# Performance work log

Measured on AMD Instinct MI355X. Metric: run time of the kernel, lower is better.

The kernel has to match this reference:

```python
import jax, jax.numpy as jnp
import numpy as np

N_NODES = 20000
N_EDGES = 100000
WIDTH = 64
KER_IN = 6
KER_HID = WIDTH // 4  # 16
DEPTH = 6


def setup_inputs() -> dict:
    key = jax.random.key(0)
    ks = jax.random.split(key, 12)
    s = lambda fan_in: 1.0 / np.sqrt(fan_in)
    return {
        "x": jax.random.normal(ks[0], (N_NODES, 1), dtype=jnp.float32),
        "edge_index": jax.random.randint(ks[1], (2, N_EDGES), 0, N_NODES, dtype=jnp.int32),
        "edge_attr": jax.random.uniform(ks[2], (N_EDGES, KER_IN), dtype=jnp.float32),
        "fc1_w": jax.random.normal(ks[3], (1, WIDTH), dtype=jnp.float32) * s(1),
        "fc1_b": jnp.zeros((WIDTH,), dtype=jnp.float32),
        "k1_w": jax.random.normal(ks[4], (KER_IN, KER_HID), dtype=jnp.float32) * s(KER_IN),
        "k1_b": jnp.zeros((KER_HID,), dtype=jnp.float32),
        "k2_w": jax.random.normal(ks[5], (KER_HID, WIDTH * WIDTH), dtype=jnp.float32) * s(KER_HID),
        "k2_b": jnp.zeros((WIDTH * WIDTH,), dtype=jnp.float32),
        "root_w": jax.random.normal(ks[6], (WIDTH, WIDTH), dtype=jnp.float32) * s(WIDTH),
        "conv_b": jnp.zeros((WIDTH,), dtype=jnp.float32),
        "fc2_w": jax.random.normal(ks[7], (WIDTH, 1), dtype=jnp.float32) * s(WIDTH),
        "fc2_b": jnp.zeros((1,), dtype=jnp.float32),
    }


def reference(x, edge_index, edge_attr, fc1_w, fc1_b, k1_w, k1_b, k2_w, k2_b,
              root_w, conv_b, fc2_w, fc2_b):
    src = edge_index[0]  # source nodes j
    dst = edge_index[1]  # target nodes i

    # fc1: lift node features [N,1] -> [N,W]
    h = x @ fc1_w + fc1_b

    # Edge-conditioned weight matrices via kernel MLP (edge_attr is layer-invariant,
    # so compute once and reuse for all DEPTH layers — identical math).
    ek = jax.nn.relu(edge_attr @ k1_w + k1_b)           # [E, W/4]
    W = (ek @ k2_w + k2_b).reshape(N_EDGES, WIDTH, WIDTH)  # [E, W, W]

    # mean aggregation denominator (in-degree, clamped to avoid div-by-zero)
    deg = jax.ops.segment_sum(jnp.ones((N_EDGES,), dtype=h.dtype), dst,
                              num_segments=N_NODES)
    denom = jnp.maximum(deg, 1.0)[:, None]               # [N,1]

    for _ in range(DEPTH):
        # per-edge matmul: msg_e = x_src[e] @ W_e
        msg = jnp.einsum('ei,eio->eo', h[src], W)        # [E, W]
        agg = jax.ops.segment_sum(msg, dst, num_segments=N_NODES) / denom
        h = jax.nn.relu(agg + h @ root_w + conv_b)       # NNConv root weight + bias, then outer ReLU

    return h @ fc2_w + fc2_b                              # [N, 1]
```

## Files before the change

kernel.cpp:

```cpp
#include <hip/hip_runtime.h>
#include <hip/hip_bf16.h>


#define NN 20000
#define NE 100000
#define WD 64
#define DEPTH 6
#define TM 15
#define LSTR 1092

typedef __attribute__((ext_vector_type(8))) short bf16x8;
typedef __attribute__((ext_vector_type(4))) float f32x4;

__device__ __forceinline__ unsigned short f2bf(float v) {
    union { float f; unsigned u; } x; x.f = v;
    unsigned r = x.u + 0x7fffu + ((x.u >> 16) & 1u);
    return (unsigned short)(r >> 16);
}
__device__ __forceinline__ float bf2f(unsigned short b) {
    union { unsigned u; float f; } x; x.u = ((unsigned)b) << 16;
    return x.f;
}

__global__ __launch_bounds__(256) void count_kernel(const int* __restrict__ ei,
                                                    int* __restrict__ outc,
                                                    int* __restrict__ inc)
{
    int e = blockIdx.x * 256 + threadIdx.x;
    if (e >= NE) return;
    atomicAdd(&outc[ei[e]], 1);
    atomicAdd(&inc[ei[NE + e]], 1);
}

__global__ __launch_bounds__(256) void scanA_kernel(const int* __restrict__ cnt,
                                                    int* __restrict__ partials)
{
    int b = blockIdx.x, t = threadIdx.x, lane = t & 63, w = t >> 6;
    int base = b * 1024 + t * 4;
    int s = 0;
#pragma unroll
    for (int i = 0; i < 4; ++i) {
        int idx = base + i;
        if (idx < 2 * NN) s += cnt[idx];
    }
#pragma unroll
    for (int off = 32; off > 0; off >>= 1) s += __shfl_down(s, off, 64);
    __shared__ int wsum[4];
    if (lane == 0) wsum[w] = s;
    __syncthreads();
    if (t == 0) partials[b] = wsum[0] + wsum[1] + wsum[2] + wsum[3];
}

__global__ __launch_bounds__(64) void scanB_kernel(const int* __restrict__ partials,
                                                   int* __restrict__ bases)
{
    int l = threadIdx.x;
    int p = (l < 40) ? partials[l] : 0;
    int v = p;
#pragma unroll
    for (int off = 1; off < 64; off <<= 1) {
        int u = __shfl_up(v, off, 64);
        if (l >= off) v += u;
    }
    if (l < 40) bases[l] = v - p;
}

__global__ __launch_bounds__(256) void scanC_kernel(const int* __restrict__ cnt,
                                                    const int* __restrict__ bases,
                                                    int* __restrict__ rps,
                                                    int* __restrict__ rpd,
                                                    float* __restrict__ invd)
{
    int b = blockIdx.x, t = threadIdx.x, lane = t & 63, w = t >> 6;
    int base = b * 1024 + t * 4;
    int v[4], s = 0;
#pragma unroll
    for (int i = 0; i < 4; ++i) {
        int idx = base + i;
        v[i] = (idx < 2 * NN) ? cnt[idx] : 0;
        s += v[i];
    }
    int tsum = s, sc = s;
#pragma unroll
    for (int off = 1; off < 64; off <<= 1) {
        int u = __shfl_up(sc, off, 64);
        if (lane >= off) sc += u;
    }
    __shared__ int wtot[4];
    if (lane == 63) wtot[w] = sc;
    __syncthreads();
    int wbase = 0;
    for (int j = 0; j < w; ++j) wbase += wtot[j];
    int run = bases[b] + wbase + sc - tsum;
#pragma unroll
    for (int i = 0; i < 4; ++i) {
        int idx = base + i;
        int e = run; run += v[i];
        if (idx < NN) {
            rps[idx] = e;
        } else if (idx < 2 * NN) {
            rpd[idx - NN] = e - NE;
            invd[idx - NN] = 1.0f / fmaxf((float)v[i], 1.0f);
        }
    }
    if (b == 0 && t == 0) { rps[NN] = NE; rpd[NN] = NE; }
}

__global__ __launch_bounds__(256) void ekfill_kernel(
    const int* __restrict__ ei, const float* __restrict__ ea,
    const float* __restrict__ k1w, const float* __restrict__ k1b,
    const int* __restrict__ rps, const int* __restrict__ rpd,
    int* __restrict__ fs, int* __restrict__ fd,
    float* __restrict__ eks, int* __restrict__ ss2sd)
{
    int e = blockIdx.x * 256 + threadIdx.x;
    if (e >= NE) return;
    int s = ei[e], d = ei[NE + e];
    float a[6];
#pragma unroll
    for (int i = 0; i < 6; ++i) a[i] = ea[e * 6 + i];
    int slot_s = rps[s] + atomicAdd(&fs[s], 1);
    int slot_d = rpd[d] + atomicAdd(&fd[d], 1);
    ss2sd[slot_s] = slot_d;
#pragma unroll
    for (int j = 0; j < 16; ++j) {
        float v = k1b[j];
#pragma unroll
        for (int i = 0; i < 6; ++i) v = fmaf(a[i], k1w[i * 16 + j], v);
        eks[(size_t)slot_s * 16 + j] = fmaxf(v, 0.f);
    }
}

__global__ __launch_bounds__(256) void gwt_kernel(
    const float* __restrict__ k2w, const float* __restrict__ k2b,
    const float* __restrict__ rootw,
    unsigned short* __restrict__ Gh, unsigned short* __restrict__ Gl)
{
    int idx = blockIdx.x * 256 + threadIdx.x;
    if (idx >= 1152 * 64) return;
    int n = idx >> 6, k = idx & 63;
    int b = n >> 6, o = n & 63;
    float g;
    if (b < 16)       g = k2w[b * 4096 + k * 64 + o];
    else if (b == 16) g = k2b[k * 64 + o];
    else              g = rootw[k * 64 + o];
    unsigned short hi = f2bf(g);
    Gh[idx] = hi;
    Gl[idx] = f2bf(g - bf2f(hi));
}

__global__ __launch_bounds__(256) void h0_kernel(
    const float* __restrict__ x, const float* __restrict__ w,
    const float* __restrict__ b,
    unsigned short* __restrict__ hhi, unsigned short* __restrict__ hlo)
{
    int idx = blockIdx.x * 256 + threadIdx.x;
    if (idx >= NN * WD) return;
    int n = idx >> 6, o = idx & 63;
    float v = fmaf(x[n], w[o], b[o]);
    unsigned short hi = f2bf(v);
    hhi[idx] = hi;
    hlo[idx] = f2bf(v - bf2f(hi));
}

__global__ __launch_bounds__(512) void fused_kernel(
    const unsigned short* __restrict__ hhi, const unsigned short* __restrict__ hlo,
    const unsigned short* __restrict__ Gh, const unsigned short* __restrict__ Gl,
    const float* __restrict__ eks, const int* __restrict__ ss2sd,
    const int* __restrict__ rps, float* __restrict__ Proot,
    float* __restrict__ msg)
{
    __shared__ __align__(16) float Pt[TM * LSTR];
    __shared__ int rb[TM + 1];
    int n0 = blockIdx.x * TM;
    int w = threadIdx.x >> 6, l = threadIdx.x & 63;
    int quad = l >> 4, lr = l & 15;
    if (threadIdx.x < TM + 1) {
        int gi = n0 + threadIdx.x;
        rb[threadIdx.x] = rps[gi > NN ? NN : gi];
    }
    int arow = n0 + lr;
    if (arow > NN - 1) arow = NN - 1;
    const bf16x8* pah = (const bf16x8*)(hhi + (size_t)arow * 64 + quad * 8);
    const bf16x8* pal = (const bf16x8*)(hlo + (size_t)arow * 64 + quad * 8);
    bf16x8 ah0 = pah[0], ah1 = pah[4];
    bf16x8 al0 = pal[0], al1 = pal[4];

    for (int st = w; st < 18; st += 8) {
        f32x4 acc[4];
#pragma unroll
        for (int t = 0; t < 4; ++t) acc[t] = (f32x4){0.f, 0.f, 0.f, 0.f};
#pragma unroll
        for (int t = 0; t < 4; ++t) {
            int brow = st * 64 + t * 16 + lr;
            const bf16x8* pbh = (const bf16x8*)(Gh + (size_t)brow * 64 + quad * 8);
            const bf16x8* pbl = (const bf16x8*)(Gl + (size_t)brow * 64 + quad * 8);
            bf16x8 bh0 = pbh[0], bh1 = pbh[4];
            bf16x8 bl0 = pbl[0], bl1 = pbl[4];
            f32x4 a = acc[t];
            a = __builtin_amdgcn_mfma_f32_16x16x32_bf16(ah0, bh0, a, 0, 0, 0);
            a = __builtin_amdgcn_mfma_f32_16x16x32_bf16(ah0, bl0, a, 0, 0, 0);
            a = __builtin_amdgcn_mfma_f32_16x16x32_bf16(al0, bh0, a, 0, 0, 0);
            a = __builtin_amdgcn_mfma_f32_16x16x32_bf16(ah1, bh1, a, 0, 0, 0);
            a = __builtin_amdgcn_mfma_f32_16x16x32_bf16(ah1, bl1, a, 0, 0, 0);
            a = __builtin_amdgcn_mfma_f32_16x16x32_bf16(al1, bh1, a, 0, 0, 0);
            acc[t] = a;
        }
        if (st < 17) {
#pragma unroll
            for (int t = 0; t < 4; ++t)
#pragma unroll
                for (int r = 0; r < 4; ++r) {
                    int row = quad * 4 + r;
                    if (row < TM)
                        Pt[row * LSTR + st * 64 + t * 16 + lr] = acc[t][r];
                }
        } else {
#pragma unroll
            for (int t = 0; t < 4; ++t)
#pragma unroll
                for (int r = 0; r < 4; ++r) {
                    int row = quad * 4 + r;
                    int gn = n0 + row;
                    if (row < TM && gn < NN)
                        Proot[(size_t)gn * 64 + t * 16 + lr] = acc[t][r];
                }
        }
    }
    __syncthreads();

    int nend = n0 + TM; if (nend > NN) nend = NN;
    int r0 = rb[0], r1 = rb[nend - n0];
    int total = r1 - r0;
    if (total <= 0) return;
    int per = (total + 7) >> 3;
    int s0 = r0 + w * per;
    int s1 = s0 + per; if (s1 > r1) s1 = r1;
    int ln = 0;
    float p[17];
    bool need = true;
    for (int s = s0; s < s1; ++s) {
        while (s >= rb[ln + 1]) { ++ln; need = true; }
        if (need) {
            const float* Pr = &Pt[ln * LSTR];
#pragma unroll
            for (int k = 0; k < 17; ++k) p[k] = Pr[k * 64 + l];
            need = false;
        }
        int su = __builtin_amdgcn_readfirstlane(s);
        const float* er = eks + (size_t)su * 16;
        f32x4 e0 = *(const f32x4*)(er);
        f32x4 e1 = *(const f32x4*)(er + 4);
        f32x4 e2 = *(const f32x4*)(er + 8);
        f32x4 e3 = *(const f32x4*)(er + 12);
        int ds = ss2sd[su];
        float ma = p[16], mb = 0.f;
        ma = fmaf(e0[0], p[0], ma);  mb = fmaf(e0[1], p[1], mb);
        ma = fmaf(e0[2], p[2], ma);  mb = fmaf(e0[3], p[3], mb);
        ma = fmaf(e1[0], p[4], ma);  mb = fmaf(e1[1], p[5], mb);
        ma = fmaf(e1[2], p[6], ma);  mb = fmaf(e1[3], p[7], mb);
        ma = fmaf(e2[0], p[8], ma);  mb = fmaf(e2[1], p[9], mb);
        ma = fmaf(e2[2], p[10], ma); mb = fmaf(e2[3], p[11], mb);
        ma = fmaf(e3[0], p[12], ma); mb = fmaf(e3[1], p[13], mb);
        ma = fmaf(e3[2], p[14], ma); mb = fmaf(e3[3], p[15], mb);
        msg[(size_t)ds * 64 + l] = ma + mb;
    }
}

__global__ __launch_bounds__(256) void agg_kernel(
    const float* __restrict__ msg, const int* __restrict__ rpd,
    const float* __restrict__ invd, const float* __restrict__ Proot,
    const float* __restrict__ convb, float* __restrict__ h,
    unsigned short* __restrict__ hhi, unsigned short* __restrict__ hlo)
{
    int i = blockIdx.x * 4 + (threadIdx.x >> 6);
    if (i >= NN) return;
    int l = threadIdx.x & 63;
    int r0 = rpd[i], r1 = rpd[i + 1];
    float a0 = 0.f, a1 = 0.f, a2 = 0.f, a3 = 0.f;
    int s = r0;
    for (; s + 3 < r1; s += 4) {
        a0 += msg[(size_t)s * 64 + l];
        a1 += msg[(size_t)(s + 1) * 64 + l];
        a2 += msg[(size_t)(s + 2) * 64 + l];
        a3 += msg[(size_t)(s + 3) * 64 + l];
    }
    for (; s < r1; ++s) a0 += msg[(size_t)s * 64 + l];
    float acc = (a0 + a1) + (a2 + a3);
    float v = fmaf(acc, invd[i], Proot[(size_t)i * 64 + l] + convb[l]);
    v = fmaxf(v, 0.f);
    int idx = i * 64 + l;
    h[idx] = v;
    unsigned short hi = f2bf(v);
    hhi[idx] = hi;
    hlo[idx] = f2bf(v - bf2f(hi));
}

__global__ __launch_bounds__(256) void out_kernel(
    const float* __restrict__ h, const float* __restrict__ fc2_w,
    const float* __restrict__ fc2_b, float* __restrict__ out)
{
    int wave = blockIdx.x * 4 + (threadIdx.x >> 6);
    int lane = threadIdx.x & 63;
    float v = h[(size_t)wave * 64 + lane] * fc2_w[lane];
#pragma unroll
    for (int off = 32; off > 0; off >>= 1) v += __shfl_down(v, off);
    if (lane == 0) out[wave] = v + fc2_b[0];
}

extern "C" void kernel_launch(void* const* d_in, const int* in_sizes, int n_in,
                              void* d_out, int out_size, void* d_ws, size_t ws_size,
                              hipStream_t stream)
{
    const float* x         = (const float*)d_in[0];
    const int*   ei        = (const int*)  d_in[1];
    const float* edge_attr = (const float*)d_in[2];
    const float* fc1_w     = (const float*)d_in[3];
    const float* fc1_b     = (const float*)d_in[4];
    const float* k1_w      = (const float*)d_in[5];
    const float* k1_b      = (const float*)d_in[6];
    const float* k2_w      = (const float*)d_in[7];
    const float* k2_b      = (const float*)d_in[8];
    const float* root_w    = (const float*)d_in[9];
    const float* conv_b    = (const float*)d_in[10];
    const float* fc2_w     = (const float*)d_in[11];
    const float* fc2_b     = (const float*)d_in[12];
    float* out = (float*)d_out;

    float* ws = (float*)d_ws;
    size_t off = 0;
    int* cnt   = (int*)(ws + off); off += 4 * NN;
    int* outc  = cnt;
    int* inc   = cnt + NN;
    int* fs    = cnt + 2 * NN;
    int* fd    = cnt + 3 * NN;
    int* rps   = (int*)(ws + off); off += 20004;
    int* rpd   = (int*)(ws + off); off += 20004;
    int* partials = (int*)(ws + off); off += 64;
    int* bases    = (int*)(ws + off); off += 64;
    int* ss2sd    = (int*)(ws + off); off += NE;
    float* invd  = ws + off; off += NN;
    float* eks   = ws + off; off += (size_t)NE * 16;
    unsigned short* Gh  = (unsigned short*)(ws + off); off += 36864;
    unsigned short* Gl  = (unsigned short*)(ws + off); off += 36864;
    unsigned short* hhi = (unsigned short*)(ws + off); off += (size_t)NN * 32;
    unsigned short* hlo = (unsigned short*)(ws + off); off += (size_t)NN * 32;
    float* h     = ws + off; off += (size_t)NN * WD;
    float* msg   = ws + off; off += (size_t)NE * WD;
    float* Proot = ws + off; off += (size_t)NN * WD;

    hipMemsetAsync(cnt, 0, 4 * NN * sizeof(int), stream);
    count_kernel<<<(NE + 255) / 256, 256, 0, stream>>>(ei, outc, inc);
    scanA_kernel<<<40, 256, 0, stream>>>(cnt, partials);
    scanB_kernel<<<1, 64, 0, stream>>>(partials, bases);
    scanC_kernel<<<40, 256, 0, stream>>>(cnt, bases, rps, rpd, invd);
    ekfill_kernel<<<(NE + 255) / 256, 256, 0, stream>>>(ei, edge_attr, k1_w, k1_b,
                                                        rps, rpd, fs, fd, eks, ss2sd);
    gwt_kernel<<<(1152 * 64 + 255) / 256, 256, 0, stream>>>(k2_w, k2_b, root_w, Gh, Gl);
    h0_kernel<<<(NN * WD + 255) / 256, 256, 0, stream>>>(x, fc1_w, fc1_b, hhi, hlo);

    int ntiles = (NN + TM - 1) / TM;
    for (int layer = 0; layer < DEPTH; ++layer) {
        fused_kernel<<<ntiles, 512, 0, stream>>>(hhi, hlo, Gh, Gl, eks, ss2sd,
                                                 rps, Proot, msg);
        agg_kernel<<<(NN + 3) / 4, 256, 0, stream>>>(msg, rpd, invd, Proot,
                                                     conv_b, h, hhi, hlo);
    }

    out_kernel<<<NN / 4, 256, 0, stream>>>(h, fc2_w, fc2_b, out);
}
```

Before: 561.8 us.

## Replace CSR gather aggregation with atomic scatter and fuse node update into conv kernel

Drops the per-edge message buffer and the separate destination-sorted aggregation kernel. Messages are now atomically added straight into a per-layer agg buffer, and the next layer's fused kernel computes the ReLU node update and bf16 hi/lo split on the fly. The h0 kernel is folded into the first layer and the final update into out_kernel. This saves the msg write/read traffic and a launch per layer, at the cost of float atomics (nondeterministic summation order), an extra memset per layer, and ping-pong buffers.

```diff
diff --git a/kernel.cpp b/kernel.cpp
--- a/kernel.cpp
+++ b/kernel.cpp
@@ -68,7 +68,6 @@
 __global__ __launch_bounds__(256) void scanC_kernel(const int* __restrict__ cnt,
                                                     const int* __restrict__ bases,
                                                     int* __restrict__ rps,
-                                                    int* __restrict__ rpd,
                                                     float* __restrict__ invd)
 {
     int b = blockIdx.x, t = threadIdx.x, lane = t & 63, w = t >> 6;
@@ -99,19 +98,17 @@
         if (idx < NN) {
             rps[idx] = e;
         } else if (idx < 2 * NN) {
-            rpd[idx - NN] = e - NE;
             invd[idx - NN] = 1.0f / fmaxf((float)v[i], 1.0f);
         }
     }
-    if (b == 0 && t == 0) { rps[NN] = NE; rpd[NN] = NE; }
+    if (b == 0 && t == 0) rps[NN] = NE;
 }
 
 __global__ __launch_bounds__(256) void ekfill_kernel(
     const int* __restrict__ ei, const float* __restrict__ ea,
     const float* __restrict__ k1w, const float* __restrict__ k1b,
-    const int* __restrict__ rps, const int* __restrict__ rpd,
-    int* __restrict__ fs, int* __restrict__ fd,
-    float* __restrict__ eks, int* __restrict__ ss2sd)
+    const int* __restrict__ rps, int* __restrict__ fs,
+    float* __restrict__ eks, int* __restrict__ dsts)
 {
     int e = blockIdx.x * 256 + threadIdx.x;
     if (e >= NE) return;
@@ -120,8 +117,7 @@
 #pragma unroll
     for (int i = 0; i < 6; ++i) a[i] = ea[e * 6 + i];
     int slot_s = rps[s] + atomicAdd(&fs[s], 1);
-    int slot_d = rpd[d] + atomicAdd(&fd[d], 1);
-    ss2sd[slot_s] = slot_d;
+    dsts[slot_s] = d;
 #pragma unroll
     for (int j = 0; j < 16; ++j) {
         float v = k1b[j];
@@ -149,26 +145,15 @@
     Gl[idx] = f2bf(g - bf2f(hi));
 }
 
-__global__ __launch_bounds__(256) void h0_kernel(
-    const float* __restrict__ x, const float* __restrict__ w,
-    const float* __restrict__ b,
-    unsigned short* __restrict__ hhi, unsigned short* __restrict__ hlo)
-{
-    int idx = blockIdx.x * 256 + threadIdx.x;
-    if (idx >= NN * WD) return;
-    int n = idx >> 6, o = idx & 63;
-    float v = fmaf(x[n], w[o], b[o]);
-    unsigned short hi = f2bf(v);
-    hhi[idx] = hi;
-    hlo[idx] = f2bf(v - bf2f(hi));
-}
-
-__global__ __launch_bounds__(512) void fused_kernel(
-    const unsigned short* __restrict__ hhi, const unsigned short* __restrict__ hlo,
+__global__ __launch_bounds__(512, 4) void fused_kernel(
+    const float* __restrict__ x, const float* __restrict__ fc1w,
+    const float* __restrict__ fc1b,
+    const float* __restrict__ aggIn, const float* __restrict__ ProotIn,
+    const float* __restrict__ invd, const float* __restrict__ convb,
     const unsigned short* __restrict__ Gh, const unsigned short* __restrict__ Gl,
-    const float* __restrict__ eks, const int* __restrict__ ss2sd,
-    const int* __restrict__ rps, float* __restrict__ Proot,
-    float* __restrict__ msg)
+    const float* __restrict__ eks, const int* __restrict__ dsts,
+    const int* __restrict__ rps,
+    float* __restrict__ ProotOut, float* __restrict__ aggOut, int first)
 {
     __shared__ __align__(16) float Pt[TM * LSTR];
     __shared__ int rb[TM + 1];
@@ -181,10 +166,58 @@
     }
     int arow = n0 + lr;
     if (arow > NN - 1) arow = NN - 1;
-    const bf16x8* pah = (const bf16x8*)(hhi + (size_t)arow * 64 + quad * 8);
-    const bf16x8* pal = (const bf16x8*)(hlo + (size_t)arow * 64 + quad * 8);
-    bf16x8 ah0 = pah[0], ah1 = pah[4];
-    bf16x8 al0 = pal[0], al1 = pal[4];
+
+    bf16x8 ah0, al0, ah1, al1;
+    if (first) {
+        float xv = x[arow];
+#pragma unroll
+        for (int half = 0; half < 2; ++half) {
+            int kb = half * 32 + quad * 8;
+            f32x4 w0 = *(const f32x4*)(fc1w + kb);
+            f32x4 w1 = *(const f32x4*)(fc1w + kb + 4);
+            f32x4 b0 = *(const f32x4*)(fc1b + kb);
+            f32x4 b1 = *(const f32x4*)(fc1b + kb + 4);
+#pragma unroll
+            for (int j = 0; j < 4; ++j) {
+                float v0 = fmaf(xv, w0[j], b0[j]);
+                float v1 = fmaf(xv, w1[j], b1[j]);
+                unsigned short h0 = f2bf(v0), h1 = f2bf(v1);
+                if (half == 0) {
+                    ah0[j] = (short)h0;     al0[j] = (short)f2bf(v0 - bf2f(h0));
+                    ah0[4 + j] = (short)h1; al0[4 + j] = (short)f2bf(v1 - bf2f(h1));
+                } else {
+                    ah1[j] = (short)h0;     al1[j] = (short)f2bf(v0 - bf2f(h0));
+                    ah1[4 + j] = (short)h1; al1[4 + j] = (short)f2bf(v1 - bf2f(h1));
+                }
+            }
+        }
+    } else {
+        float iv = invd[arow];
+        size_t rbase = (size_t)arow * 64;
+#pragma unroll
+        for (int half = 0; half < 2; ++half) {
+            int kb = half * 32 + quad * 8;
+            f32x4 g0 = *(const f32x4*)(aggIn + rbase + kb);
+            f32x4 g1 = *(const f32x4*)(aggIn + rbase + kb + 4);
+            f32x4 p0 = *(const f32x4*)(ProotIn + rbase + kb);
+            f32x4 p1 = *(const f32x4*)(ProotIn + rbase + kb + 4);
+            f32x4 c0 = *(const f32x4*)(convb + kb);
+            f32x4 c1 = *(const f32x4*)(convb + kb + 4);
+#pragma unroll
+            for (int j = 0; j < 4; ++j) {
+                float v0 = fmaxf(fmaf(g0[j], iv, p0[j] + c0[j]), 0.f);
+                float v1 = fmaxf(fmaf(g1[j], iv, p1[j] + c1[j]), 0.f);
+                unsigned short h0 = f2bf(v0), h1 = f2bf(v1);
+                if (half == 0) {
+                    ah0[j] = (short)h0;     al0[j] = (short)f2bf(v0 - bf2f(h0));
+                    ah0[4 + j] = (short)h1; al0[4 + j] = (short)f2bf(v1 - bf2f(h1));
+                } else {
+                    ah1[j] = (short)h0;     al1[j] = (short)f2bf(v0 - bf2f(h0));
+                    ah1[4 + j] = (short)h1; al1[4 + j] = (short)f2bf(v1 - bf2f(h1));
+                }
+            }
+        }
+    }
 
     for (int st = w; st < 18; st += 8) {
         f32x4 acc[4];
@@ -223,89 +256,64 @@
                     int row = quad * 4 + r;
                     int gn = n0 + row;
                     if (row < TM && gn < NN)
-                        Proot[(size_t)gn * 64 + t * 16 + lr] = acc[t][r];
+                        ProotOut[(size_t)gn * 64 + t * 16 + lr] = acc[t][r];
                 }
         }
     }
     __syncthreads();
 
     int nend = n0 + TM; if (nend > NN) nend = NN;
-    int r0 = rb[0], r1 = rb[nend - n0];
+    int tmeff = nend - n0;
+    int r0 = rb[0], r1 = rb[tmeff];
     int total = r1 - r0;
     if (total <= 0) return;
     int per = (total + 7) >> 3;
     int s0 = r0 + w * per;
     int s1 = s0 + per; if (s1 > r1) s1 = r1;
-    int ln = 0;
-    float p[17];
-    bool need = true;
-    for (int s = s0; s < s1; ++s) {
-        while (s >= rb[ln + 1]) { ++ln; need = true; }
-        if (need) {
-            const float* Pr = &Pt[ln * LSTR];
-#pragma unroll
-            for (int k = 0; k < 17; ++k) p[k] = Pr[k * 64 + l];
-            need = false;
-        }
-        int su = __builtin_amdgcn_readfirstlane(s);
-        const float* er = eks + (size_t)su * 16;
-        f32x4 e0 = *(const f32x4*)(er);
-        f32x4 e1 = *(const f32x4*)(er + 4);
-        f32x4 e2 = *(const f32x4*)(er + 8);
-        f32x4 e3 = *(const f32x4*)(er + 12);
-        int ds = ss2sd[su];
-        float ma = p[16], mb = 0.f;
-        ma = fmaf(e0[0], p[0], ma);  mb = fmaf(e0[1], p[1], mb);
-        ma = fmaf(e0[2], p[2], ma);  mb = fmaf(e0[3], p[3], mb);
-        ma = fmaf(e1[0], p[4], ma);  mb = fmaf(e1[1], p[5], mb);
-        ma = fmaf(e1[2], p[6], ma);  mb = fmaf(e1[3], p[7], mb);
-        ma = fmaf(e2[0], p[8], ma);  mb = fmaf(e2[1], p[9], mb);
-        ma = fmaf(e2[2], p[10], ma); mb = fmaf(e2[3], p[11], mb);
-        ma = fmaf(e3[0], p[12], ma); mb = fmaf(e3[1], p[13], mb);
-        ma = fmaf(e3[2], p[14], ma); mb = fmaf(e3[3], p[15], mb);
-        msg[(size_t)ds * 64 + l] = ma + mb;
-    }
-}
-
-__global__ __launch_bounds__(256) void agg_kernel(
-    const float* __restrict__ msg, const int* __restrict__ rpd,
-    const float* __restrict__ invd, const float* __restrict__ Proot,
-    const float* __restrict__ convb, float* __restrict__ h,
-    unsigned short* __restrict__ hhi, unsigned short* __restrict__ hlo)
-{
-    int i = blockIdx.x * 4 + (threadIdx.x >> 6);
-    if (i >= NN) return;
+    for (int ln = 0; ln < tmeff && s0 < s1; ++ln) {
+        int lo = s0 > rb[ln] ? s0 : rb[ln];
+        int hi = s1 < rb[ln + 1] ? s1 : rb[ln + 1];
+        if (lo >= hi) continue;
+        float p[17];
+        const float* Pr = &Pt[ln * LSTR];
+#pragma unroll
+        for (int k = 0; k < 17; ++k) p[k] = Pr[k * 64 + l];
+        for (int s = lo; s < hi; ++s) {
+            int su = __builtin_amdgcn_readfirstlane(s);
+            const float* er = eks + (size_t)su * 16;
+            f32x4 e0 = *(const f32x4*)(er);
+            f32x4 e1 = *(const f32x4*)(er + 4);
+            f32x4 e2 = *(const f32x4*)(er + 8);
+            f32x4 e3 = *(const f32x4*)(er + 12);
+            int d = dsts[su];
+            float ma = p[16], mb = 0.f;
+            ma = fmaf(e0[0], p[0], ma);  mb = fmaf(e0[1], p[1], mb);
+            ma = fmaf(e0[2], p[2], ma);  mb = fmaf(e0[3], p[3], mb);
+            ma = fmaf(e1[0], p[4], ma);  mb = fmaf(e1[1], p[5], mb);
+            ma = fmaf(e1[2], p[6], ma);  mb = fmaf(e1[3], p[7], mb);
+            ma = fmaf(e2[0], p[8], ma);  mb = fmaf(e2[1], p[9], mb);
+            ma = fmaf(e2[2], p[10], ma); mb = fmaf(e2[3], p[11], mb);
+            ma = fmaf(e3[0], p[12], ma); mb = fmaf(e3[1], p[13], mb);
+            ma = fmaf(e3[2], p[14], ma); mb = fmaf(e3[3], p[15], mb);
+            atomicAdd(&aggOut[(size_t)d * 64 + l], ma + mb);
+        }
+    }
+}
+
+__global__ __launch_bounds__(256) void out_kernel(
+    const float* __restrict__ agg, const float* __restrict__ Proot,
+    const float* __restrict__ invd, const float* __restrict__ convb,
+    const float* __restrict__ fc2_w, const float* __restrict__ fc2_b,
+    float* __restrict__ out)
+{
+    int n = blockIdx.x * 4 + (threadIdx.x >> 6);
     int l = threadIdx.x & 63;
-    int r0 = rpd[i], r1 = rpd[i + 1];
-    float a0 = 0.f, a1 = 0.f, a2 = 0.f, a3 = 0.f;
-    int s = r0;
-    for (; s + 3 < r1; s += 4) {
-        a0 += msg[(size_t)s * 64 + l];
-        a1 += msg[(size_t)(s + 1) * 64 + l];
-        a2 += msg[(size_t)(s + 2) * 64 + l];
-        a3 += msg[(size_t)(s + 3) * 64 + l];
-    }
-    for (; s < r1; ++s) a0 += msg[(size_t)s * 64 + l];
-    float acc = (a0 + a1) + (a2 + a3);
-    float v = fmaf(acc, invd[i], Proot[(size_t)i * 64 + l] + convb[l]);
-    v = fmaxf(v, 0.f);
-    int idx = i * 64 + l;
-    h[idx] = v;
-    unsigned short hi = f2bf(v);
-    hhi[idx] = hi;
-    hlo[idx] = f2bf(v - bf2f(hi));
-}
-
-__global__ __launch_bounds__(256) void out_kernel(
-    const float* __restrict__ h, const float* __restrict__ fc2_w,
-    const float* __restrict__ fc2_b, float* __restrict__ out)
-{
-    int wave = blockIdx.x * 4 + (threadIdx.x >> 6);
-    int lane = threadIdx.x & 63;
-    float v = h[(size_t)wave * 64 + lane] * fc2_w[lane];
+    float v = fmaf(agg[(size_t)n * 64 + l], invd[n],
+                   Proot[(size_t)n * 64 + l] + convb[l]);
+    v = fmaxf(v, 0.f) * fc2_w[l];
 #pragma unroll
     for (int off = 32; off > 0; off >>= 1) v += __shfl_down(v, off);
-    if (lane == 0) out[wave] = v + fc2_b[0];
+    if (l == 0) out[n] = v + fc2_b[0];
 }
 
 extern "C" void kernel_launch(void* const* d_in, const int* in_sizes, int n_in,
@@ -329,43 +337,46 @@
 
     float* ws = (float*)d_ws;
     size_t off = 0;
-    int* cnt   = (int*)(ws + off); off += 4 * NN;
+    int* cnt   = (int*)(ws + off); off += 3 * NN;
     int* outc  = cnt;
     int* inc   = cnt + NN;
     int* fs    = cnt + 2 * NN;
-    int* fd    = cnt + 3 * NN;
     int* rps   = (int*)(ws + off); off += 20004;
-    int* rpd   = (int*)(ws + off); off += 20004;
     int* partials = (int*)(ws + off); off += 64;
     int* bases    = (int*)(ws + off); off += 64;
-    int* ss2sd    = (int*)(ws + off); off += NE;
+    int* dsts  = (int*)(ws + off); off += NE;
     float* invd  = ws + off; off += NN;
     float* eks   = ws + off; off += (size_t)NE * 16;
     unsigned short* Gh  = (unsigned short*)(ws + off); off += 36864;
     unsigned short* Gl  = (unsigned short*)(ws + off); off += 36864;
-    unsigned short* hhi = (unsigned short*)(ws + off); off += (size_t)NN * 32;
-    unsigned short* hlo = (unsigned short*)(ws + off); off += (size_t)NN * 32;
-    float* h     = ws + off; off += (size_t)NN * WD;
-    float* msg   = ws + off; off += (size_t)NE * WD;
-    float* Proot = ws + off; off += (size_t)NN * WD;
-
-    hipMemsetAsync(cnt, 0, 4 * NN * sizeof(int), stream);
+    float* aggA   = ws + off; off += (size_t)NN * WD;
+    float* aggB   = ws + off; off += (size_t)NN * WD;
+    float* ProotA = ws + off; off += (size_t)NN * WD;
+    float* ProotB = ws + off; off += (size_t)NN * WD;
+
+    hipMemsetAsync(cnt, 0, 3 * NN * sizeof(int), stream);
     count_kernel<<<(NE + 255) / 256, 256, 0, stream>>>(ei, outc, inc);
     scanA_kernel<<<40, 256, 0, stream>>>(cnt, partials);
     scanB_kernel<<<1, 64, 0, stream>>>(partials, bases);
-    scanC_kernel<<<40, 256, 0, stream>>>(cnt, bases, rps, rpd, invd);
+    scanC_kernel<<<40, 256, 0, stream>>>(cnt, bases, rps, invd);
     ekfill_kernel<<<(NE + 255) / 256, 256, 0, stream>>>(ei, edge_attr, k1_w, k1_b,
-                                                        rps, rpd, fs, fd, eks, ss2sd);
+                                                        rps, fs, eks, dsts);
     gwt_kernel<<<(1152 * 64 + 255) / 256, 256, 0, stream>>>(k2_w, k2_b, root_w, Gh, Gl);
-    h0_kernel<<<(NN * WD + 255) / 256, 256, 0, stream>>>(x, fc1_w, fc1_b, hhi, hlo);
 
     int ntiles = (NN + TM - 1) / TM;
+    float* aggIn = aggB;   float* aggOut = aggA;
+    float* prIn  = ProotB; float* prOut  = ProotA;
     for (int layer = 0; layer < DEPTH; ++layer) {
-        fused_kernel<<<ntiles, 512, 0, stream>>>(hhi, hlo, Gh, Gl, eks, ss2sd,
-                                                 rps, Proot, msg);
-        agg_kernel<<<(NN + 3) / 4, 256, 0, stream>>>(msg, rpd, invd, Proot,
-                                                     conv_b, h, hhi, hlo);
-    }
-
-    out_kernel<<<NN / 4, 256, 0, stream>>>(h, fc2_w, fc2_b, out);
-}
+        hipMemsetAsync(aggOut, 0, (size_t)NN * WD * sizeof(float), stream);
+        fused_kernel<<<ntiles, 512, 0, stream>>>(x, fc1_w, fc1_b,
+                                                 aggIn, prIn, invd, conv_b,
+                                                 Gh, Gl, eks, dsts, rps,
+                                                 prOut, aggOut, layer == 0 ? 1 : 0);
+        float* t;
+        t = aggIn; aggIn = aggOut; aggOut = t;
+        t = prIn;  prIn  = prOut;  prOut  = t;
+    }
+
+    out_kernel<<<NN / 4, 256, 0, stream>>>(aggIn, prIn, invd, conv_b,
+                                           fc2_w, fc2_b, out);
+}
```

Measured after the change: 569.0 us. Within noise of the previous version (+1.3%).
